# Optimization experiments

Measured on AMD Instinct MI355X. Metric: run time of the kernel, lower is better.

The kernel has to match this reference:

```python
import jax, jax.numpy as jnp
import numpy as np

GAMMA = 0.1   # gl.gamma
BIG = 1e10    # stand-in for +inf in the DP border (keeps grads NaN-free)


def _softdtw(D, gamma=GAMMA):
    """Soft-DTW value for a batch of cost matrices D: [B, T, T] -> [B].
    R[i,j] = D[i,j] + softmin_gamma(R[i-1,j-1], R[i-1,j], R[i,j-1]).
    Vectorized over the batch; sequential DP over rows (outer scan) and
    columns (inner scan), matching the reference recurrence exactly.
    """
    B, T, _ = D.shape
    dt = D.dtype
    # R[0, :] = [0, inf, inf, ...]  (length T+1, padded border)
    prev = jnp.concatenate([jnp.zeros((B, 1), dt), jnp.full((B, T), BIG, dt)], axis=1)

    def col_step(r_left, xs):
        d, r_diag, r_up = xs  # each [B]
        stacked = jnp.stack([r_diag, r_up, r_left])  # [3, B]
        r = d - gamma * jax.nn.logsumexp(-stacked / gamma, axis=0)
        return r, r

    def row_step(prev_row, d_row):  # prev_row [B, T+1], d_row [B, T]
        xs = (d_row.T, prev_row[:, :-1].T, prev_row[:, 1:].T)  # each [T, B]
        _, rows = jax.lax.scan(col_step, jnp.full((B,), BIG, dt), xs)  # [T, B]
        new_row = jnp.concatenate([jnp.full((B, 1), BIG, dt), rows.T], axis=1)
        return new_row, None

    final_row, _ = jax.lax.scan(row_step, prev, jnp.swapaxes(D, 0, 1))
    return final_row[:, -1]  # R[T, T]


def setup_inputs() -> dict:
    key = jax.random.key(0)
    n_class, n_support, n_query, t, c = 20, 5, 25, 32, 2048
    n = n_class * (n_support + n_query)
    inp = jax.random.normal(key, (n, t, c), jnp.float32)
    # episode labels, grouped per class (as produced by an episodic sampler)
    target = jnp.repeat(jnp.arange(n_class, dtype=jnp.int32), n_support + n_query)
    return {"inp": inp, "target": target, "n_support": n_support, "n_class": n_class}


def reference(inp, target, n_support, n_class):
    n, t, c = inp.shape
    per_class = n // n_class
    n_query = per_class - n_support

    # group samples by class (stable sort == torch.nonzero(target.eq(c)) ordering)
    order = jnp.argsort(target, stable=True)
    grouped = inp[order].reshape(n_class, per_class, t, c)
    z_proto = grouped[:, :n_support].mean(axis=1)                 # [m, t, c]
    zq = grouped[:, n_support:].reshape(n_class * n_query, t, c)  # [nq, t, c]

    # pairwise squared-Euclidean frame costs (no [nq*m, t, c] expansion)
    x2 = jnp.sum(zq * zq, axis=-1)          # [nq, t]
    y2 = jnp.sum(z_proto * z_proto, axis=-1)  # [m, t]
    xy = jnp.einsum('nic,mjc->nmij', zq, z_proto)  # [nq, m, t, t]
    cost_xy = x2[:, None, :, None] + y2[None, :, None, :] - 2.0 * xy
    nq, m = cost_xy.shape[:2]
    d_xy = _softdtw(cost_xy.reshape(nq * m, t, t)).reshape(nq, m)

    # normalization terms: D(x,x), D(y,y)
    cxx = x2[:, :, None] + x2[:, None, :] - 2.0 * jnp.einsum('nic,njc->nij', zq, zq)
    cyy = y2[:, :, None] + y2[:, None, :] - 2.0 * jnp.einsum('mic,mjc->mij', z_proto, z_proto)
    d_xx = _softdtw(cxx)  # [nq]
    d_yy = _softdtw(cyy)  # [m]
    dist = d_xy - 0.5 * (d_xx[:, None] + d_yy[None, :])  # [nq, m]

    log_p_y = jax.nn.log_softmax(-dist, axis=1).reshape(n_class, n_query, n_class)
    tgt = jnp.broadcast_to(jnp.arange(n_class)[:, None, None], (n_class, n_query, 1))
    batch_loss = -jnp.take_along_axis(log_p_y, tgt, axis=2).reshape(-1)
    loss_val = batch_loss.mean()
    y_hat = jnp.argmax(log_p_y, axis=2)
    acc_val = (y_hat == tgt[..., 0]).astype(jnp.float32).mean()
    return loss_val, acc_val, batch_loss
```

## Files before the change

### kernel.cpp

```cpp
#include <hip/hip_runtime.h>

#define T 32
#define C 2048
#define NTOT 600
#define NCLASS 20
#define NSUP 5
#define PER 30
#define NQPC 25
#define NQ 500
#define NQROWS (NQ * T)
#define NPROWS (NCLASS * T)
#define GAMMA 0.1f
#define INVG 10.0f
#define BIG 1e10f
#define NMM (NQ * NCLASS + NQ + NCLASS)
#define GEMM_BLKS 625
#define SYRK_BLKS_PAD 136
#define SAMP_STRIDE 8192
#define STAGE_BLKS_A 2000
#define STAGE_BLKS_B 80
#define LDS_PITCH 33

typedef __fp16 half8 __attribute__((ext_vector_type(8)));
typedef __fp16 half4 __attribute__((ext_vector_type(4)));
typedef float f32x4 __attribute__((ext_vector_type(4)));

__global__ __launch_bounds__(640) void sort_kernel(const int* __restrict__ target,
                                                   int* __restrict__ order,
                                                   int* __restrict__ qsrc) {
    __shared__ int tgt[NTOT];
    __shared__ int offs[NCLASS];
    __shared__ int ordl[NTOT];
    int tid = threadIdx.x;
    if (tid < NTOT) tgt[tid] = target[tid];
    __syncthreads();
    if (tid < NCLASS) {
        int o = 0;
        for (int i = 0; i < NTOT; i++) o += (tgt[i] < tid) ? 1 : 0;
        offs[tid] = o;
    }
    __syncthreads();
    if (tid < NTOT) {
        int c = tgt[tid];
        int rank = 0;
        for (int k = 0; k < NTOT; k++) rank += (k < tid && tgt[k] == c) ? 1 : 0;
        ordl[offs[c] + rank] = tid;
    }
    __syncthreads();
    if (tid < NTOT) order[tid] = ordl[tid];
    if (tid < NQ) qsrc[tid] = ordl[(tid / NQPC) * PER + NSUP + (tid % NQPC)];
}

__global__ __launch_bounds__(256) void stage_kernel(const float* __restrict__ inp,
                                                    const int* __restrict__ qsrc,
                                                    const int* __restrict__ order,
                                                    half8* __restrict__ Ah,
                                                    half8* __restrict__ Bh) {
    __shared__ half8 lds[4][16][LDS_PITCH];
    int tid = threadIdx.x;
    int lane = tid & 63, w = tid >> 6;
    int bid = blockIdx.x;
    bool isA = bid < STAGE_BLKS_A;
    int b = isA ? bid : bid - STAGE_BLKS_A;
    int rowblk = b >> 1, half = b & 1;
    int row0 = rowblk * 16;
    int colbase = half * 1024 + w * 256;
    if (isA) {
        int q = row0 >> 5, rowin0 = row0 & 31;
        const float* sbase = inp + (size_t)qsrc[q] * (T * C) + (size_t)rowin0 * C +
                             colbase + lane * 4;
#pragma unroll
        for (int rr = 0; rr < 16; rr++) {
            float4 v = *(const float4*)(sbase + (size_t)rr * C);
            half4 hv = {(__fp16)v.x, (__fp16)v.y, (__fp16)v.z, (__fp16)v.w};
            ((half4*)&lds[w][rr][0])[lane] = hv;
        }
        __syncthreads();
        int chunkbase = half * 128 + w * 32;
        half8* dst = Ah + (size_t)q * SAMP_STRIDE + rowin0;
#pragma unroll
        for (int c = 0; c < 8; c++) {
            int idx = c * 64 + lane;
            int ch = idx >> 4, row = idx & 15;
            dst[(size_t)(chunkbase + ch) * 32 + row] = lds[w][row][ch];
        }
    } else {
#pragma unroll
        for (int rr = 0; rr < 16; rr++) {
            int rg = row0 + rr;
            int cls = rg >> 5, trow = rg & 31;
            const float* base = inp + (size_t)trow * C + colbase + lane * 4;
            float4 a = *(const float4*)(base + (size_t)order[cls * PER + 0] * (T * C));
            float4 b4 = *(const float4*)(base + (size_t)order[cls * PER + 1] * (T * C));
            float4 c = *(const float4*)(base + (size_t)order[cls * PER + 2] * (T * C));
            float4 d = *(const float4*)(base + (size_t)order[cls * PER + 3] * (T * C));
            float4 e = *(const float4*)(base + (size_t)order[cls * PER + 4] * (T * C));
            float4 m;
            m.x = (a.x + b4.x + c.x + d.x + e.x) * 0.2f;
            m.y = (a.y + b4.y + c.y + d.y + e.y) * 0.2f;
            m.z = (a.z + b4.z + c.z + d.z + e.z) * 0.2f;
            m.w = (a.w + b4.w + c.w + d.w + e.w) * 0.2f;
            half4 hv = {(__fp16)m.x, (__fp16)m.y, (__fp16)m.z, (__fp16)m.w};
            ((half4*)&lds[w][rr][0])[lane] = hv;
        }
        __syncthreads();
        int chunkbase = half * 128 + w * 32;
#pragma unroll
        for (int c = 0; c < 8; c++) {
            int idx = c * 64 + lane;
            int ch = idx >> 4, row = idx & 15;
            Bh[(size_t)(chunkbase + ch) * NPROWS + row0 + row] = lds[w][row][ch];
        }
    }
}

__global__ __launch_bounds__(256) void gemm_syrk_kernel(const half8* __restrict__ Ah,
                                                        const half8* __restrict__ Bh,
                                                        float* __restrict__ xy,
                                                        float* __restrict__ gxx,
                                                        float* __restrict__ gyy) {
    int tid = threadIdx.x, lane = tid & 63, wid = tid >> 6;
    int o = blockIdx.x;
    int g = lane >> 4, r = lane & 15;
    if (o < SYRK_BLKS_PAD) {
        int ww = o * 4 + wid;
        if (ww >= NQ + NCLASS) return;
        f32x4 acc[2][2];
        f32x4 zero = {0.f, 0.f, 0.f, 0.f};
        acc[0][0] = zero; acc[0][1] = zero; acc[1][0] = zero; acc[1][1] = zero;
        if (ww < NQ) {
            const half8* p = Ah + (size_t)ww * SAMP_STRIDE + g * 32 + r;
            float* outp = gxx + (size_t)ww * (T * T);
            for (int t = 0; t < C / 32; t++) {
                half8 h0 = p[0], h1 = p[16];
                p += 128;
                acc[0][0] = __builtin_amdgcn_mfma_f32_16x16x32_f16(h0, h0, acc[0][0], 0, 0, 0);
                acc[0][1] = __builtin_amdgcn_mfma_f32_16x16x32_f16(h0, h1, acc[0][1], 0, 0, 0);
                acc[1][0] = __builtin_amdgcn_mfma_f32_16x16x32_f16(h1, h0, acc[1][0], 0, 0, 0);
                acc[1][1] = __builtin_amdgcn_mfma_f32_16x16x32_f16(h1, h1, acc[1][1], 0, 0, 0);
            }
#pragma unroll
            for (int mi = 0; mi < 2; mi++)
#pragma unroll
                for (int ni = 0; ni < 2; ni++)
#pragma unroll
                    for (int j = 0; j < 4; j++)
                        outp[(mi * 16 + g * 4 + j) * T + ni * 16 + r] = acc[mi][ni][j];
        } else {
            int row0 = (ww - NQ) * 32;
            float* outp = gyy + (size_t)(ww - NQ) * (T * T);
            for (int t = 0; t < C / 32; t++) {
                size_t base = (size_t)(t * 4 + g) * NPROWS + row0 + r;
                half8 h0 = Bh[base], h1 = Bh[base + 16];
                acc[0][0] = __builtin_amdgcn_mfma_f32_16x16x32_f16(h0, h0, acc[0][0], 0, 0, 0);
                acc[0][1] = __builtin_amdgcn_mfma_f32_16x16x32_f16(h0, h1, acc[0][1], 0, 0, 0);
                acc[1][0] = __builtin_amdgcn_mfma_f32_16x16x32_f16(h1, h0, acc[1][0], 0, 0, 0);
                acc[1][1] = __builtin_amdgcn_mfma_f32_16x16x32_f16(h1, h1, acc[1][1], 0, 0, 0);
            }
#pragma unroll
            for (int mi = 0; mi < 2; mi++)
#pragma unroll
                for (int ni = 0; ni < 2; ni++)
#pragma unroll
                    for (int j = 0; j < 4; j++)
                        outp[(mi * 16 + g * 4 + j) * T + ni * 16 + r] = acc[mi][ni][j];
        }
        return;
    }
    int oo = o - SYRK_BLKS_PAD;
    int xcd = oo & 7, slot = oo >> 3;
    int v = (xcd < 1 ? xcd * 79 : 79 + (xcd - 1) * 78) + slot;
    int bm = v / 5, bn = v % 5;
    int wr = wid >> 1, wc = wid & 1;
    int m0 = bm * 128 + wr * 64, n0 = bn * 128 + wc * 64;
    int q0 = m0 >> 5;
    int p0 = n0 >> 5;
    const half8* pA0 = Ah + (size_t)q0 * SAMP_STRIDE + g * 32 + r;
    const half8* pA1 = pA0 + SAMP_STRIDE;
    const half8* pB = Bh + (size_t)g * NPROWS + n0 + r;
    f32x4 acc[4][4];
    f32x4 zero = {0.f, 0.f, 0.f, 0.f};
#pragma unroll
    for (int mi = 0; mi < 4; mi++)
#pragma unroll
        for (int ni = 0; ni < 4; ni++) acc[mi][ni] = zero;
#pragma unroll 2
    for (int t = 0; t < C / 32; t++) {
        half8 ah[4], bh[4];
        ah[0] = pA0[0];
        ah[1] = pA0[16];
        ah[2] = pA1[0];
        ah[3] = pA1[16];
#pragma unroll
        for (int i = 0; i < 4; i++) bh[i] = pB[i * 16];
        pA0 += 128;
        pA1 += 128;
        pB += 4 * NPROWS;
#pragma unroll
        for (int mi = 0; mi < 4; mi++)
#pragma unroll
            for (int ni = 0; ni < 4; ni++)
                acc[mi][ni] = __builtin_amdgcn_mfma_f32_16x16x32_f16(ah[mi], bh[ni], acc[mi][ni], 0, 0, 0);
    }
#pragma unroll
    for (int mi = 0; mi < 4; mi++)
#pragma unroll
        for (int ni = 0; ni < 4; ni++) {
            float* ob = xy + ((size_t)(q0 + (mi >> 1)) * NCLASS + p0 + (ni >> 1)) * 1024 +
                        ((mi & 1) * 16 + g * 4) * 32 + (ni & 1) * 16 + r;
#pragma unroll
            for (int j = 0; j < 4; j++)
                ob[j * 32] = acc[mi][ni][j];
        }
}

__global__ __launch_bounds__(256) void softdtw_wave_kernel(
        const float* __restrict__ xy, const float* __restrict__ gxx,
        const float* __restrict__ gyy, float* __restrict__ dxy,
        float* __restrict__ dxx, float* __restrict__ dyy) {
    int tid = threadIdx.x;
    int j = tid & 31;
    int mm = blockIdx.x * 8 + (tid >> 5);
    bool valid = mm < NMM;
    int mmc = valid ? mm : 0;
    const float* rbase;
    const float* cbase;
    const float* cptr;
    float* outp;
    if (mmc < NQ * NCLASS) {
        int q = mmc / NCLASS, m = mmc % NCLASS;
        rbase = gxx + (size_t)q * (T * T);
        cbase = gyy + (size_t)m * (T * T);
        cptr = xy + (size_t)mmc * (T * T);
        outp = dxy + mmc;
    } else if (mmc < NQ * NCLASS + NQ) {
        int i = mmc - NQ * NCLASS;
        rbase = gxx + (size_t)i * (T * T);
        cbase = rbase;
        cptr = rbase;
        outp = dxx + i;
    } else {
        int i = mmc - NQ * NCLASS - NQ;
        rbase = gyy + (size_t)i * (T * T);
        cbase = rbase;
        cptr = rbase;
        outp = dyy + i;
    }
    float cjv = cbase[j * 33];
    float xreg = rbase[j * 33];
    float my_prev = BIG, my_prev2 = BIG;
    int ip = 0 - j; ip = ip < 0 ? 0 : (ip > 31 ? 31 : ip);
    float nxt_xy = cptr[ip * T + j];
    for (int k = 0; k < 63; k++) {
        float cur_xy = nxt_xy;
        int in = k + 1 - j; in = in < 0 ? 0 : (in > 31 ? 31 : in);
        nxt_xy = cptr[in * T + j];
        float lp = __shfl_up(my_prev, 1, 32);
        float dg = __shfl_up(my_prev2, 1, 32);
        if (j == 0) { lp = BIG; dg = (k == 0) ? 0.f : BIG; }
        float up = my_prev;
        int i = k - j;
        float ai = __shfl(xreg, i & 31, 32);
        float d = ai + cjv - 2.0f * cur_xy;
        float mn = fminf(dg, fminf(up, lp));
        float ssum = __expf((mn - dg) * INVG) + __expf((mn - up) * INVG) +
                     __expf((mn - lp) * INVG);
        float r = d + mn - GAMMA * __logf(ssum);
        bool active = (i >= 0) && (i < 32);
        my_prev2 = my_prev;
        my_prev = active ? r : my_prev;
    }
    if (j == 31 && valid) *outp = my_prev;
}

__global__ __launch_bounds__(512) void finalize_kernel(const float* __restrict__ dxy,
                                                       const float* __restrict__ dxx,
                                                       const float* __restrict__ dyy,
                                                       float* __restrict__ out) {
    __shared__ float sl[512];
    __shared__ float sa[512];
    int q = threadIdx.x;
    float bl = 0.f, fl = 0.f;
    if (q < NQ) {
        float dxxq = dxx[q];
        int cq = q / NQPC;
        float dd[NCLASS];
#pragma unroll
        for (int m = 0; m < NCLASS; m++)
            dd[m] = dxy[q * NCLASS + m] - 0.5f * (dxxq + dyy[m]);
        float best = dd[0];
        int bi = 0;
#pragma unroll
        for (int m = 1; m < NCLASS; m++) {
            if (dd[m] < best) { best = dd[m]; bi = m; }
        }
        float s = 0.f;
        float dcq = dd[0];
#pragma unroll
        for (int m = 0; m < NCLASS; m++) {
            s += __expf(best - dd[m]);
            if (m == cq) dcq = dd[m];
        }
        float lse = __logf(s) - best;
        bl = dcq + lse;
        out[2 + q] = bl;
        fl = (bi == cq) ? 1.f : 0.f;
    }
    sl[threadIdx.x] = bl;
    sa[threadIdx.x] = fl;
    __syncthreads();
    for (int off = 256; off; off >>= 1) {
        if (threadIdx.x < off) {
            sl[threadIdx.x] += sl[threadIdx.x + off];
            sa[threadIdx.x] += sa[threadIdx.x + off];
        }
        __syncthreads();
    }
    if (threadIdx.x == 0) {
        out[0] = sl[0] / (float)NQ;
        out[1] = sa[0] / (float)NQ;
    }
}

extern "C" void kernel_launch(void* const* d_in, const int* in_sizes, int n_in,
                              void* d_out, int out_size, void* d_ws, size_t ws_size,
                              hipStream_t stream) {
    const float* inp = (const float*)d_in[0];
    const int* target = (const int*)d_in[1];
    float* out = (float*)d_out;
    char* ws = (char*)d_ws;

    size_t off = 0;
    auto carve = [&](size_t bytes) {
        void* p = ws + off;
        off = (off + bytes + 255) & ~(size_t)255;
        return p;
    };
    int* order = (int*)carve(NTOT * sizeof(int));
    int* qsrc = (int*)carve(NQ * sizeof(int));
    float* xy = (float*)carve((size_t)NQ * NCLASS * T * T * sizeof(float));
    float* gxx = (float*)carve((size_t)NQ * T * T * sizeof(float));
    float* gyy = (float*)carve((size_t)NCLASS * T * T * sizeof(float));
    float* dxy = (float*)carve((size_t)NQ * NCLASS * sizeof(float));
    float* dxx = (float*)carve((size_t)NQ * sizeof(float));
    float* dyy = (float*)carve((size_t)NCLASS * sizeof(float));
    half8* Ah = (half8*)carve((size_t)NQ * SAMP_STRIDE * 16);
    half8* Bh = (half8*)carve((size_t)(C / 8) * NPROWS * 16);
    (void)ws_size;

    sort_kernel<<<1, 640, 0, stream>>>(target, order, qsrc);
    stage_kernel<<<STAGE_BLKS_A + STAGE_BLKS_B, 256, 0, stream>>>(inp, qsrc, order, Ah, Bh);
    gemm_syrk_kernel<<<SYRK_BLKS_PAD + GEMM_BLKS, 256, 0, stream>>>(Ah, Bh, xy, gxx, gyy);
    softdtw_wave_kernel<<<(NMM + 7) / 8, 256, 0, stream>>>(xy, gxx, gyy, dxy, dxx, dyy);
    finalize_kernel<<<1, 512, 0, stream>>>(dxy, dxx, dyy, out);
}
```

Measured before the change: 172.0 us.

## Fuse cross-pair soft-DTW into GEMM epilogue and compute squared norms during staging

Row squared norms are now computed during staging from the fp16-rounded values via wave reductions into per-row partials, so the pairwise path no longer reads diagonals of the Gram matrices. The GEMM epilogue moves each wave's accumulator tiles into shared memory and runs the wavefront soft-DTW recurrence for its query/prototype pairs there. This removes the round trip through global memory for the 500x20x32x32 fp32 cross-cost matrix. In exchange the GEMM blocks take on the serial 63-step DP, which lengthens their tail and adds shared-memory pressure; the self-distance DP stays in its own smaller kernel.

New measurement: 164.2 us. 1.05x faster.

```diff
diff --git a/kernel.cpp b/kernel.cpp
--- a/kernel.cpp
+++ b/kernel.cpp
@@ -13,7 +13,7 @@
 #define GAMMA 0.1f
 #define INVG 10.0f
 #define BIG 1e10f
-#define NMM (NQ * NCLASS + NQ + NCLASS)
+#define NSELF (NQ + NCLASS)
 #define GEMM_BLKS 625
 #define SYRK_BLKS_PAD 136
 #define SAMP_STRIDE 8192
@@ -55,7 +55,9 @@
                                                     const int* __restrict__ qsrc,
                                                     const int* __restrict__ order,
                                                     half8* __restrict__ Ah,
-                                                    half8* __restrict__ Bh) {
+                                                    half8* __restrict__ Bh,
+                                                    float* __restrict__ x2part,
+                                                    float* __restrict__ y2part) {
     __shared__ half8 lds[4][16][LDS_PITCH];
     int tid = threadIdx.x;
     int lane = tid & 63, w = tid >> 6;
@@ -65,6 +67,7 @@
     int rowblk = b >> 1, half = b & 1;
     int row0 = rowblk * 16;
     int colbase = half * 1024 + w * 256;
+    int pidx = half * 4 + w;
     if (isA) {
         int q = row0 >> 5, rowin0 = row0 & 31;
         const float* sbase = inp + (size_t)qsrc[q] * (T * C) + (size_t)rowin0 * C +
@@ -74,6 +77,11 @@
             float4 v = *(const float4*)(sbase + (size_t)rr * C);
             half4 hv = {(__fp16)v.x, (__fp16)v.y, (__fp16)v.z, (__fp16)v.w};
             ((half4*)&lds[w][rr][0])[lane] = hv;
+            float fx = (float)hv[0], fy = (float)hv[1], fz = (float)hv[2], fw = (float)hv[3];
+            float s = fx * fx + fy * fy + fz * fz + fw * fw;
+#pragma unroll
+            for (int d = 1; d < 64; d <<= 1) s += __shfl_xor(s, d);
+            if (lane == 0) x2part[(size_t)(row0 + rr) * 8 + pidx] = s;
         }
         __syncthreads();
         int chunkbase = half * 128 + w * 32;
@@ -102,6 +110,11 @@
             m.w = (a.w + b4.w + c.w + d.w + e.w) * 0.2f;
             half4 hv = {(__fp16)m.x, (__fp16)m.y, (__fp16)m.z, (__fp16)m.w};
             ((half4*)&lds[w][rr][0])[lane] = hv;
+            float fx = (float)hv[0], fy = (float)hv[1], fz = (float)hv[2], fw = (float)hv[3];
+            float s = fx * fx + fy * fy + fz * fz + fw * fw;
+#pragma unroll
+            for (int dd = 1; dd < 64; dd <<= 1) s += __shfl_xor(s, dd);
+            if (lane == 0) y2part[(size_t)rg * 8 + pidx] = s;
         }
         __syncthreads();
         int chunkbase = half * 128 + w * 32;
@@ -116,15 +129,18 @@
 
 __global__ __launch_bounds__(256) void gemm_syrk_kernel(const half8* __restrict__ Ah,
                                                         const half8* __restrict__ Bh,
-                                                        float* __restrict__ xy,
+                                                        const float* __restrict__ x2part,
+                                                        const float* __restrict__ y2part,
+                                                        float* __restrict__ dxy,
                                                         float* __restrict__ gxx,
                                                         float* __restrict__ gyy) {
+    __shared__ float dmat[4][2][32][32];
     int tid = threadIdx.x, lane = tid & 63, wid = tid >> 6;
     int o = blockIdx.x;
     int g = lane >> 4, r = lane & 15;
     if (o < SYRK_BLKS_PAD) {
         int ww = o * 4 + wid;
-        if (ww >= NQ + NCLASS) return;
+        if (ww >= NSELF) return;
         f32x4 acc[2][2];
         f32x4 zero = {0.f, 0.f, 0.f, 0.f};
         acc[0][0] = zero; acc[0][1] = zero; acc[1][0] = zero; acc[1][1] = zero;
@@ -202,75 +218,97 @@
             for (int ni = 0; ni < 4; ni++)
                 acc[mi][ni] = __builtin_amdgcn_mfma_f32_16x16x32_f16(ah[mi], bh[ni], acc[mi][ni], 0, 0, 0);
     }
-#pragma unroll
-    for (int mi = 0; mi < 4; mi++)
-#pragma unroll
-        for (int ni = 0; ni < 4; ni++) {
-            float* ob = xy + ((size_t)(q0 + (mi >> 1)) * NCLASS + p0 + (ni >> 1)) * 1024 +
-                        ((mi & 1) * 16 + g * 4) * 32 + (ni & 1) * 16 + r;
-#pragma unroll
-            for (int j = 0; j < 4; j++)
-                ob[j * 32] = acc[mi][ni][j];
-        }
-}
-
-__global__ __launch_bounds__(256) void softdtw_wave_kernel(
-        const float* __restrict__ xy, const float* __restrict__ gxx,
-        const float* __restrict__ gyy, float* __restrict__ dxy,
+    int jj = lane & 31;
+    int hh = lane >> 5;
+    float xreg = 0.f;
+    {
+        const float* xp = x2part + ((size_t)(q0 + hh) * 32 + jj) * 8;
+#pragma unroll
+        for (int p = 0; p < 8; p++) xreg += xp[p];
+    }
+#pragma unroll
+    for (int pp = 0; pp < 2; pp++) {
+        __syncthreads();
+#pragma unroll
+        for (int qi = 0; qi < 2; qi++)
+#pragma unroll
+            for (int m2 = 0; m2 < 2; m2++)
+#pragma unroll
+                for (int nn = 0; nn < 2; nn++)
+#pragma unroll
+                    for (int j = 0; j < 4; j++)
+                        dmat[wid][qi][m2 * 16 + g * 4 + j][nn * 16 + r] =
+                            acc[qi * 2 + m2][pp * 2 + nn][j];
+        __syncthreads();
+        float cjv = 0.f;
+        {
+            const float* yp = y2part + ((size_t)(p0 + pp) * 32 + jj) * 8;
+#pragma unroll
+            for (int p = 0; p < 8; p++) cjv += yp[p];
+        }
+        const float* cm = &dmat[wid][hh][0][0];
+        float my_prev = BIG, my_prev2 = BIG;
+        int ip = 0 - jj; ip = ip < 0 ? 0 : ip;
+        float nxt = cm[ip * 32 + jj];
+        for (int k = 0; k < 63; k++) {
+            float cur = nxt;
+            int in = k + 1 - jj; in = in < 0 ? 0 : (in > 31 ? 31 : in);
+            nxt = cm[in * 32 + jj];
+            float lp = __shfl_up(my_prev, 1, 32);
+            float dg = __shfl_up(my_prev2, 1, 32);
+            if (jj == 0) { lp = BIG; dg = (k == 0) ? 0.f : BIG; }
+            float up = my_prev;
+            int i = k - jj;
+            float ai = __shfl(xreg, i & 31, 32);
+            float d = ai + cjv - 2.0f * cur;
+            float mn = fminf(dg, fminf(up, lp));
+            float ssum = __expf((mn - dg) * INVG) + __expf((mn - up) * INVG) +
+                         __expf((mn - lp) * INVG);
+            float rv = d + mn - GAMMA * __logf(ssum);
+            bool act = (i >= 0) && (i < 32);
+            my_prev2 = my_prev;
+            my_prev = act ? rv : my_prev;
+        }
+        if (jj == 31) dxy[(size_t)(q0 + hh) * NCLASS + p0 + pp] = my_prev;
+    }
+}
+
+__global__ __launch_bounds__(256) void softdtw_self_kernel(
+        const float* __restrict__ gxx, const float* __restrict__ gyy,
         float* __restrict__ dxx, float* __restrict__ dyy) {
     int tid = threadIdx.x;
-    int j = tid & 31;
+    int jj = tid & 31;
     int mm = blockIdx.x * 8 + (tid >> 5);
-    bool valid = mm < NMM;
+    bool valid = mm < NSELF;
     int mmc = valid ? mm : 0;
-    const float* rbase;
-    const float* cbase;
-    const float* cptr;
-    float* outp;
-    if (mmc < NQ * NCLASS) {
-        int q = mmc / NCLASS, m = mmc % NCLASS;
-        rbase = gxx + (size_t)q * (T * T);
-        cbase = gyy + (size_t)m * (T * T);
-        cptr = xy + (size_t)mmc * (T * T);
-        outp = dxy + mmc;
-    } else if (mmc < NQ * NCLASS + NQ) {
-        int i = mmc - NQ * NCLASS;
-        rbase = gxx + (size_t)i * (T * T);
-        cbase = rbase;
-        cptr = rbase;
-        outp = dxx + i;
-    } else {
-        int i = mmc - NQ * NCLASS - NQ;
-        rbase = gyy + (size_t)i * (T * T);
-        cbase = rbase;
-        cptr = rbase;
-        outp = dyy + i;
-    }
-    float cjv = cbase[j * 33];
-    float xreg = rbase[j * 33];
+    const float* base = (mmc < NQ) ? gxx + (size_t)mmc * (T * T)
+                                   : gyy + (size_t)(mmc - NQ) * (T * T);
+    float* outp = (mmc < NQ) ? dxx + mmc : dyy + (mmc - NQ);
+    float cjv = base[jj * 33];
+    float xreg = cjv;
     float my_prev = BIG, my_prev2 = BIG;
-    int ip = 0 - j; ip = ip < 0 ? 0 : (ip > 31 ? 31 : ip);
-    float nxt_xy = cptr[ip * T + j];
+    int ip = 0 - jj; ip = ip < 0 ? 0 : ip;
+    float nxt = base[ip * T + jj];
     for (int k = 0; k < 63; k++) {
-        float cur_xy = nxt_xy;
-        int in = k + 1 - j; in = in < 0 ? 0 : (in > 31 ? 31 : in);
-        nxt_xy = cptr[in * T + j];
+        float cur = nxt;
+        int in = k + 1 - jj; in = in < 0 ? 0 : (in > 31 ? 31 : in);
+        nxt = base[in * T + jj];
         float lp = __shfl_up(my_prev, 1, 32);
         float dg = __shfl_up(my_prev2, 1, 32);
-        if (j == 0) { lp = BIG; dg = (k == 0) ? 0.f : BIG; }
+        if (jj == 0) { lp = BIG; dg = (k == 0) ? 0.f : BIG; }
         float up = my_prev;
-        int i = k - j;
+        int i = k - jj;
         float ai = __shfl(xreg, i & 31, 32);
-        float d = ai + cjv - 2.0f * cur_xy;
+        float d = ai + cjv - 2.0f * cur;
         float mn = fminf(dg, fminf(up, lp));
         float ssum = __expf((mn - dg) * INVG) + __expf((mn - up) * INVG) +
                      __expf((mn - lp) * INVG);
-        float r = d + mn - GAMMA * __logf(ssum);
-        bool active = (i >= 0) && (i < 32);
+        float rv = d + mn - GAMMA * __logf(ssum);
+        bool act = (i >= 0) && (i < 32);
         my_prev2 = my_prev;
-        my_prev = active ? r : my_prev;
-    }
-    if (j == 31 && valid) *outp = my_prev;
+        my_prev = act ? rv : my_prev;
+    }
+    if (jj == 31 && valid) *outp = my_prev;
 }
 
 __global__ __launch_bounds__(512) void finalize_kernel(const float* __restrict__ dxy,
@@ -338,7 +376,8 @@
     };
     int* order = (int*)carve(NTOT * sizeof(int));
     int* qsrc = (int*)carve(NQ * sizeof(int));
-    float* xy = (float*)carve((size_t)NQ * NCLASS * T * T * sizeof(float));
+    float* x2part = (float*)carve((size_t)NQROWS * 8 * sizeof(float));
+    float* y2part = (float*)carve((size_t)NPROWS * 8 * sizeof(float));
     float* gxx = (float*)carve((size_t)NQ * T * T * sizeof(float));
     float* gyy = (float*)carve((size_t)NCLASS * T * T * sizeof(float));
     float* dxy = (float*)carve((size_t)NQ * NCLASS * sizeof(float));
@@ -349,8 +388,10 @@
     (void)ws_size;
 
     sort_kernel<<<1, 640, 0, stream>>>(target, order, qsrc);
-    stage_kernel<<<STAGE_BLKS_A + STAGE_BLKS_B, 256, 0, stream>>>(inp, qsrc, order, Ah, Bh);
-    gemm_syrk_kernel<<<SYRK_BLKS_PAD + GEMM_BLKS, 256, 0, stream>>>(Ah, Bh, xy, gxx, gyy);
-    softdtw_wave_kernel<<<(NMM + 7) / 8, 256, 0, stream>>>(xy, gxx, gyy, dxy, dxx, dyy);
+    stage_kernel<<<STAGE_BLKS_A + STAGE_BLKS_B, 256, 0, stream>>>(inp, qsrc, order, Ah, Bh,
+                                                                  x2part, y2part);
+    gemm_syrk_kernel<<<SYRK_BLKS_PAD + GEMM_BLKS, 256, 0, stream>>>(Ah, Bh, x2part, y2part,
+                                                                    dxy, gxx, gyy);
+    softdtw_self_kernel<<<(NSELF + 7) / 8, 256, 0, stream>>>(gxx, gyy, dxx, dyy);
     finalize_kernel<<<1, 512, 0, stream>>>(dxy, dxx, dyy, out);
 }
```
